# Performance work log

Measured on AMD Instinct MI355X. Metric: run time of the kernel, lower is better.

## Reference

```python
import jax, jax.numpy as jnp
import numpy as np

N_NODES = 10000
N_EDGES = 160000
D_IN = 512
D_HID = 1024

def setup_inputs() -> dict:
    key = jax.random.key(0)
    ks = jax.random.split(key, 8)
    feat = jax.random.normal(ks[0], (N_NODES, D_IN), dtype=jnp.float32)
    W1 = jax.random.normal(ks[1], (D_IN, D_HID), dtype=jnp.float32) * (1.0 / np.sqrt(D_IN))
    b1 = jnp.zeros((D_HID,), dtype=jnp.float32)
    W2 = jax.random.normal(ks[2], (D_HID, D_IN), dtype=jnp.float32) * (1.0 / np.sqrt(D_HID))
    b2 = jnp.zeros((D_IN,), dtype=jnp.float32)
    eps = jnp.zeros((1,), dtype=jnp.float32)
    src = jax.random.randint(ks[3], (N_EDGES,), 0, N_NODES, dtype=jnp.int32)
    dst = jax.random.randint(ks[4], (N_EDGES,), 0, N_NODES, dtype=jnp.int32)
    return {"feat": feat, "W1": W1, "b1": b1, "W2": W2, "b2": b2,
            "eps": eps, "src": src, "dst": dst}

def reference(feat, W1, b1, W2, b2, eps, src, dst):
    # message passing: copy src feature along each edge, sum-reduce at dst
    msgs = feat[src]                                   # [E, D_IN] gather
    neigh = jax.ops.segment_sum(msgs, dst, num_segments=feat.shape[0])  # [N, D_IN]
    # GIN combine: (1 + eps) * self + sum(neighbors)
    rst = (1.0 + eps[0]) * feat + neigh
    # apply_func: 2-layer MLP with ReLU
    h = jnp.maximum(rst @ W1 + b1, 0.0)
    h = h @ W2 + b2
    # identity residual (in_dim == out_dim)
    return h + feat
```

## Files before the change

kernel.cpp:

```cpp
#include <hip/hip_runtime.h>

typedef unsigned short u16;
typedef unsigned int u32;
typedef __bf16 bf16x8 __attribute__((ext_vector_type(8)));
typedef float f32x4 __attribute__((ext_vector_type(4)));

#define N_NODES 10000
#define N_EDGES 160000
#define D_IN 512
#define D_HID 1024

#define AS1 __attribute__((address_space(1)))
#define AS3 __attribute__((address_space(3)))

__device__ __forceinline__ u16 f2bf(float f) {
    union { float f; u32 u; } v; v.f = f;
    return (u16)((v.u + 0x7fffu + ((v.u >> 16) & 1u)) >> 16);
}
__device__ __forceinline__ float b2f(u32 h) {
    union { u32 u; float f; } v; v.u = h << 16; return v.f;
}

__global__ void hist_k(const int* __restrict__ dst, int* __restrict__ counts) {
    int e = blockIdx.x * 256 + threadIdx.x;
    if (e < N_EDGES) atomicAdd(&counts[dst[e]], 1);
}

__global__ __launch_bounds__(1024) void scan_k(const int* __restrict__ counts,
                                               int* __restrict__ offs,
                                               int* __restrict__ cursor) {
    __shared__ int wpre[16];
    int t = threadIdx.x, l = t & 63, w = t >> 6;
    int base = t * 10;
    int c[10];
    int lsum = 0;
#pragma unroll
    for (int i = 0; i < 10; i++) {
        int idx = base + i;
        c[i] = (idx < N_NODES) ? counts[idx] : 0;
        lsum += c[i];
    }
    int sc = lsum;
#pragma unroll
    for (int d = 1; d < 64; d <<= 1) {
        int v = __shfl_up(sc, d);
        if (l >= d) sc += v;
    }
    __shared__ int wsum[16];
    if (l == 63) wsum[w] = sc;
    __syncthreads();
    if (w == 0 && l < 16) {
        int v = wsum[l];
        int p = v;
#pragma unroll
        for (int d = 1; d < 16; d <<= 1) {
            int u = __shfl_up(p, d);
            if (l >= d) p += u;
        }
        wpre[l] = p - v;
    }
    __syncthreads();
    int run = wpre[w] + sc - lsum;
#pragma unroll
    for (int i = 0; i < 10; i++) {
        int idx = base + i;
        if (idx < N_NODES) { offs[idx] = run; cursor[idx] = run; run += c[i]; }
    }
    if (t == 1023) offs[N_NODES] = wpre[15] + sc;
}

__global__ void reorder_k(const int* __restrict__ src, const int* __restrict__ dst,
                          int* __restrict__ cursor, int* __restrict__ ssrc) {
    int e = blockIdx.x * 256 + threadIdx.x;
    if (e >= N_EDGES) return;
    int d = dst[e];
    int pos = atomicAdd(&cursor[d], 1);
    ssrc[pos] = src[e];
}

__global__ void cvt_bf16_k(const float* __restrict__ in, u16* __restrict__ out, int n) {
    int i = (blockIdx.x * 256 + threadIdx.x) * 8;
    if (i >= n) return;
    float4 a = *(const float4*)(in + i);
    float4 b = *(const float4*)(in + i + 4);
    uint4 o;
    o.x = (u32)f2bf(a.x) | ((u32)f2bf(a.y) << 16);
    o.y = (u32)f2bf(a.z) | ((u32)f2bf(a.w) << 16);
    o.z = (u32)f2bf(b.x) | ((u32)f2bf(b.y) << 16);
    o.w = (u32)f2bf(b.z) | ((u32)f2bf(b.w) << 16);
    *(uint4*)(out + i) = o;
}

__global__ void transw_k(const float* __restrict__ W1, u16* __restrict__ w1t,
                         const float* __restrict__ W2, u16* __restrict__ w2t) {
    __shared__ float tile[32][33];
    int b = blockIdx.x;
    const float* W; u16* WT; int K, N, nt;
    if (b < 512) { W = W1; WT = w1t; K = D_IN;  N = D_HID; nt = 32; }
    else         { b -= 512; W = W2; WT = w2t; K = D_HID; N = D_IN;  nt = 16; }
    int n0 = (b % nt) * 32, k0 = (b / nt) * 32;
    int tx = threadIdx.x, ty = threadIdx.y;
#pragma unroll
    for (int i = 0; i < 32; i += 8)
        tile[ty + i][tx] = W[(size_t)(k0 + ty + i) * N + n0 + tx];
    __syncthreads();
#pragma unroll
    for (int i = 0; i < 32; i += 8)
        WT[(size_t)(n0 + ty + i) * K + k0 + tx] = f2bf(tile[tx][ty + i]);
}

__global__ __launch_bounds__(128) void gather_k(const float* __restrict__ feat,
                                                const u16* __restrict__ featb,
                                                const float* __restrict__ eps,
                                                const int* __restrict__ offs,
                                                const int* __restrict__ ssrc,
                                                u16* __restrict__ out) {
    int n = (blockIdx.x * 128 + threadIdx.x) >> 6;
    int l = threadIdx.x & 63;
    if (n >= N_NODES) return;
    int beg = offs[n], end = offs[n + 1];
    float s = 1.0f + eps[0];
    float4 s0 = *(const float4*)(feat + (size_t)n * D_IN + l * 8);
    float4 s1 = *(const float4*)(feat + (size_t)n * D_IN + l * 8 + 4);
    float acc[8] = { s * s0.x, s * s0.y, s * s0.z, s * s0.w,
                     s * s1.x, s * s1.y, s * s1.z, s * s1.w };
    int e = beg;
    for (; e + 4 <= end; e += 4) {
        int i0 = ssrc[e], i1 = ssrc[e + 1], i2 = ssrc[e + 2], i3 = ssrc[e + 3];
        uint4 v0 = *(const uint4*)(featb + (size_t)i0 * D_IN + l * 8);
        uint4 v1 = *(const uint4*)(featb + (size_t)i1 * D_IN + l * 8);
        uint4 v2 = *(const uint4*)(featb + (size_t)i2 * D_IN + l * 8);
        uint4 v3 = *(const uint4*)(featb + (size_t)i3 * D_IN + l * 8);
#define ACC4(v) \
        acc[0] += b2f(v.x & 0xffffu); acc[1] += b2f(v.x >> 16); \
        acc[2] += b2f(v.y & 0xffffu); acc[3] += b2f(v.y >> 16); \
        acc[4] += b2f(v.z & 0xffffu); acc[5] += b2f(v.z >> 16); \
        acc[6] += b2f(v.w & 0xffffu); acc[7] += b2f(v.w >> 16);
        ACC4(v0) ACC4(v1) ACC4(v2) ACC4(v3)
    }
    for (; e < end; e++) {
        int i0 = ssrc[e];
        uint4 v0 = *(const uint4*)(featb + (size_t)i0 * D_IN + l * 8);
        ACC4(v0)
    }
#undef ACC4
    uint4 o;
    o.x = (u32)f2bf(acc[0]) | ((u32)f2bf(acc[1]) << 16);
    o.y = (u32)f2bf(acc[2]) | ((u32)f2bf(acc[3]) << 16);
    o.z = (u32)f2bf(acc[4]) | ((u32)f2bf(acc[5]) << 16);
    o.w = (u32)f2bf(acc[6]) | ((u32)f2bf(acc[7]) << 16);
    *(uint4*)(out + (size_t)n * D_IN + l * 8) = o;
}

template <int EPI>
__global__ __launch_bounds__(256) void gemm_k(const u16* __restrict__ A,
                                              const u16* __restrict__ BT,
                                              const float* __restrict__ bias,
                                              const float* __restrict__ feat,
                                              void* __restrict__ Cout,
                                              int M, int N, int K) {
    __shared__ __bf16 sA[128 * 64];
    __shared__ __bf16 sB[128 * 64];
    const int row0 = blockIdx.y * 128;
    const int col0 = blockIdx.x * 128;
    const int t = threadIdx.x;
    const int w = t >> 6, l = t & 63;
    const int wm = (w >> 1) * 64, wn = (w & 1) * 64;
    const int lr = l & 15;
    const int lq = l >> 4;

    const u16* pA[4];
    const u16* pB[4];
    __bf16* lA[4];
    __bf16* lB[4];
    {
        int rloc = w * 32 + (l >> 3);
        int gch8 = (((l & 7) ^ (l >> 3)) * 8);
#pragma unroll
        for (int q = 0; q < 4; q++) {
            int ar = row0 + rloc + q * 8; if (ar > M - 1) ar = M - 1;
            pA[q] = A + (size_t)ar * K + gch8;
            int br = col0 + rloc + q * 8;
            pB[q] = BT + (size_t)br * K + gch8;
            lA[q] = sA + (w * 32 + q * 8) * 64;
            lB[q] = sB + (w * 32 + q * 8) * 64;
        }
    }
    const int fo = ((lq ^ (lr & 7)) * 8);

    f32x4 acc[4][4] = {};

    for (int k0 = 0; k0 < K; k0 += 64) {
        __syncthreads();
#pragma unroll
        for (int q = 0; q < 4; q++) {
            __builtin_amdgcn_global_load_lds((const AS1 void*)(pA[q] + k0),
                                             (AS3 void*)lA[q], 16, 0, 0);
            __builtin_amdgcn_global_load_lds((const AS1 void*)(pB[q] + k0),
                                             (AS3 void*)lB[q], 16, 0, 0);
        }
        __syncthreads();
#pragma unroll
        for (int kk = 0; kk < 64; kk += 32) {
            const int fx = fo ^ kk;
            bf16x8 fa[4], fb[4];
#pragma unroll
            for (int i = 0; i < 4; i++)
                fa[i] = *(const bf16x8*)(sA + (wm + i * 16 + lr) * 64 + fx);
#pragma unroll
            for (int j = 0; j < 4; j++)
                fb[j] = *(const bf16x8*)(sB + (wn + j * 16 + lr) * 64 + fx);
#pragma unroll
            for (int i = 0; i < 4; i++)
#pragma unroll
                for (int j = 0; j < 4; j++)
                    acc[i][j] = __builtin_amdgcn_mfma_f32_16x16x32_bf16(
                        fa[i], fb[j], acc[i][j], 0, 0, 0);
        }
    }

#pragma unroll
    for (int i = 0; i < 4; i++) {
        int rowb = row0 + wm + i * 16 + lq * 4;
#pragma unroll
        for (int j = 0; j < 4; j++) {
            int col = col0 + wn + j * 16 + lr;
            float bv = bias[col];
#pragma unroll
            for (int r = 0; r < 4; r++) {
                int rr = rowb + r;
                if (rr < M) {
                    float v = acc[i][j][r] + bv;
                    if (EPI == 0) {
                        v = fmaxf(v, 0.0f);
                        ((u16*)Cout)[(size_t)rr * N + col] = f2bf(v);
                    } else {
                        v += feat[(size_t)rr * N + col];
                        ((float*)Cout)[(size_t)rr * N + col] = v;
                    }
                }
            }
        }
    }
}

extern "C" void kernel_launch(void* const* d_in, const int* in_sizes, int n_in,
                              void* d_out, int out_size, void* d_ws, size_t ws_size,
                              hipStream_t stream) {
    const float* feat = (const float*)d_in[0];
    const float* W1   = (const float*)d_in[1];
    const float* b1   = (const float*)d_in[2];
    const float* W2   = (const float*)d_in[3];
    const float* b2   = (const float*)d_in[4];
    const float* eps  = (const float*)d_in[5];
    const int*   src  = (const int*)d_in[6];
    const int*   dst  = (const int*)d_in[7];
    float* out = (float*)d_out;

    char* ws = (char*)d_ws;
    u16* rst_b16 = (u16*)(ws);
    u16* h_b16   = (u16*)(ws + 10240000);
    u16* featb   = (u16*)(ws + 30720000);
    u16* w1t     = (u16*)(ws + 40960000);
    u16* w2t     = (u16*)(ws + 42008576);
    int* counts  = (int*)(ws + 43057152);
    int* offs    = (int*)(ws + 43097152);
    int* cursor  = (int*)(ws + 43137160);
    int* ssrc    = (int*)(ws + 43177160);

    const int NE = N_NODES * D_IN;

    hipMemsetAsync(counts, 0, N_NODES * sizeof(int), stream);
    hist_k<<<(N_EDGES + 255) / 256, 256, 0, stream>>>(dst, counts);
    scan_k<<<1, 1024, 0, stream>>>(counts, offs, cursor);
    reorder_k<<<(N_EDGES + 255) / 256, 256, 0, stream>>>(src, dst, cursor, ssrc);

    cvt_bf16_k<<<NE / 8 / 256, 256, 0, stream>>>(feat, featb, NE);
    transw_k<<<1024, dim3(32, 8), 0, stream>>>(W1, w1t, W2, w2t);

    gather_k<<<(N_NODES + 1) / 2, 128, 0, stream>>>(feat, featb, eps, offs, ssrc, rst_b16);

    const int MT = (N_NODES + 127) / 128;
    gemm_k<0><<<dim3(D_HID / 128, MT), 256, 0, stream>>>(rst_b16, w1t, b1, nullptr,
                                                         (void*)h_b16, N_NODES, D_HID, D_IN);
    gemm_k<1><<<dim3(D_IN / 128, MT), 256, 0, stream>>>(h_b16, w2t, b2, feat,
                                                        (void*)out, N_NODES, D_IN, D_HID);
}
```

Before: 206.4 us.

## Double-buffer LDS tiles in GEMM to overlap global loads with MFMA

The GEMM kernel now keeps two LDS buffers per operand. It issues the global_load_lds for the next K tile before computing on the current one, and uses a partial vmcnt wait plus barriers in place of the two full syncthreads per iteration. The goal is to hide global memory latency behind the MFMA work. In exchange, LDS use per block doubles, which can lower occupancy, and the last iteration issues a redundant reload of the same tile.

```diff
diff --git a/kernel.cpp b/kernel.cpp
--- a/kernel.cpp
+++ b/kernel.cpp
@@ -159,8 +159,8 @@
                                               const float* __restrict__ feat,
                                               void* __restrict__ Cout,
                                               int M, int N, int K) {
-    __shared__ __bf16 sA[128 * 64];
-    __shared__ __bf16 sB[128 * 64];
+    __shared__ __bf16 sA[2][128 * 64];
+    __shared__ __bf16 sB[2][128 * 64];
     const int row0 = blockIdx.y * 128;
     const int col0 = blockIdx.x * 128;
     const int t = threadIdx.x;
@@ -171,8 +171,7 @@
 
     const u16* pA[4];
     const u16* pB[4];
-    __bf16* lA[4];
-    __bf16* lB[4];
+    int loff[4];
     {
         int rloc = w * 32 + (l >> 3);
         int gch8 = (((l & 7) ^ (l >> 3)) * 8);
@@ -182,34 +181,40 @@
             pA[q] = A + (size_t)ar * K + gch8;
             int br = col0 + rloc + q * 8;
             pB[q] = BT + (size_t)br * K + gch8;
-            lA[q] = sA + (w * 32 + q * 8) * 64;
-            lB[q] = sB + (w * 32 + q * 8) * 64;
+            loff[q] = (w * 32 + q * 8) * 64;
         }
     }
     const int fo = ((lq ^ (lr & 7)) * 8);
 
     f32x4 acc[4][4] = {};
 
-    for (int k0 = 0; k0 < K; k0 += 64) {
-        __syncthreads();
+    auto STAGE = [&](int buf, int kk0) {
 #pragma unroll
         for (int q = 0; q < 4; q++) {
-            __builtin_amdgcn_global_load_lds((const AS1 void*)(pA[q] + k0),
-                                             (AS3 void*)lA[q], 16, 0, 0);
-            __builtin_amdgcn_global_load_lds((const AS1 void*)(pB[q] + k0),
-                                             (AS3 void*)lB[q], 16, 0, 0);
-        }
-        __syncthreads();
+            __builtin_amdgcn_global_load_lds((const AS1 void*)(pA[q] + kk0),
+                                             (AS3 void*)(&sA[buf][loff[q]]), 16, 0, 0);
+            __builtin_amdgcn_global_load_lds((const AS1 void*)(pB[q] + kk0),
+                                             (AS3 void*)(&sB[buf][loff[q]]), 16, 0, 0);
+        }
+    };
+
+    STAGE(0, 0);
+    int cur = 0;
+    for (int k0 = 0; k0 < K; k0 += 64, cur ^= 1) {
+        int kn = (k0 + 64 < K) ? (k0 + 64) : k0;
+        STAGE(cur ^ 1, kn);
+        asm volatile("s_waitcnt vmcnt(8)" ::: "memory");
+        __builtin_amdgcn_s_barrier();
 #pragma unroll
         for (int kk = 0; kk < 64; kk += 32) {
             const int fx = fo ^ kk;
             bf16x8 fa[4], fb[4];
 #pragma unroll
             for (int i = 0; i < 4; i++)
-                fa[i] = *(const bf16x8*)(sA + (wm + i * 16 + lr) * 64 + fx);
+                fa[i] = *(const bf16x8*)(&sA[cur][0] + (wm + i * 16 + lr) * 64 + fx);
 #pragma unroll
             for (int j = 0; j < 4; j++)
-                fb[j] = *(const bf16x8*)(sB + (wn + j * 16 + lr) * 64 + fx);
+                fb[j] = *(const bf16x8*)(&sB[cur][0] + (wn + j * 16 + lr) * 64 + fx);
 #pragma unroll
             for (int i = 0; i < 4; i++)
 #pragma unroll
@@ -217,6 +222,7 @@
                     acc[i][j] = __builtin_amdgcn_mfma_f32_16x16x32_bf16(
                         fa[i], fb[j], acc[i][j], 0, 0, 0);
         }
+        __builtin_amdgcn_s_barrier();
     }
 
 #pragma unroll
```

Result: slower. 221.8 us (+7.4%).

## Double-buffer GEMM LDS tiles via register prefetch and remap blocks per XCD

Applied to the files above, without the earlier changes.

Replaces the direct global-to-LDS loads in the GEMM with register-staged prefetch into a double-buffered shared-memory tile, so the next K tile's global loads overlap the current tile's MFMA work and one barrier per iteration is removed. It also remaps workgroup indices so consecutive tiles land on the same XCD for better L2 reuse, and sets a 2-blocks-per-CU occupancy hint. The trade-off is double the LDS use (64 KB per block) and more register pressure from the staged uint4 values. The swizzle moves from the global address to the LDS write offset.

```diff
diff --git a/kernel.cpp b/kernel.cpp
--- a/kernel.cpp
+++ b/kernel.cpp
@@ -9,9 +9,6 @@
 #define N_EDGES 160000
 #define D_IN 512
 #define D_HID 1024
-
-#define AS1 __attribute__((address_space(1)))
-#define AS3 __attribute__((address_space(3)))
 
 __device__ __forceinline__ u16 f2bf(float f) {
     union { float f; u32 u; } v; v.f = f;
@@ -153,16 +150,24 @@
 }
 
 template <int EPI>
-__global__ __launch_bounds__(256) void gemm_k(const u16* __restrict__ A,
-                                              const u16* __restrict__ BT,
-                                              const float* __restrict__ bias,
-                                              const float* __restrict__ feat,
-                                              void* __restrict__ Cout,
-                                              int M, int N, int K) {
-    __shared__ __bf16 sA[128 * 64];
-    __shared__ __bf16 sB[128 * 64];
-    const int row0 = blockIdx.y * 128;
-    const int col0 = blockIdx.x * 128;
+__global__ __launch_bounds__(256, 2) void gemm_k(const u16* __restrict__ A,
+                                                 const u16* __restrict__ BT,
+                                                 const float* __restrict__ bias,
+                                                 const float* __restrict__ feat,
+                                                 void* __restrict__ Cout,
+                                                 int M, int N, int K) {
+    __shared__ __bf16 sA[2][128 * 64];
+    __shared__ __bf16 sB[2][128 * 64];
+
+    const int NX = gridDim.x;
+    const int nwg = NX * gridDim.y;
+    const int flat = blockIdx.y * NX + blockIdx.x;
+    const int qq = nwg >> 3, rr8 = nwg & 7;
+    const int xcd = flat & 7, idx = flat >> 3;
+    const int L = (xcd < rr8 ? xcd * (qq + 1) : rr8 * (qq + 1) + (xcd - rr8) * qq) + idx;
+    const int row0 = (L / NX) * 128;
+    const int col0 = (L % NX) * 128;
+
     const int t = threadIdx.x;
     const int w = t >> 6, l = t & 63;
     const int wm = (w >> 1) * 64, wn = (w & 1) * 64;
@@ -171,51 +176,75 @@
 
     const u16* pA[4];
     const u16* pB[4];
-    __bf16* lA[4];
-    __bf16* lB[4];
+    u32 ldso[4];
     {
         int rloc = w * 32 + (l >> 3);
-        int gch8 = (((l & 7) ^ (l >> 3)) * 8);
+        int gch8 = (l & 7) * 8;
+        int slot = ((l & 7) ^ (l >> 3)) * 8;
 #pragma unroll
         for (int q = 0; q < 4; q++) {
             int ar = row0 + rloc + q * 8; if (ar > M - 1) ar = M - 1;
             pA[q] = A + (size_t)ar * K + gch8;
             int br = col0 + rloc + q * 8;
             pB[q] = BT + (size_t)br * K + gch8;
-            lA[q] = sA + (w * 32 + q * 8) * 64;
-            lB[q] = sB + (w * 32 + q * 8) * 64;
+            ldso[q] = (u32)(((rloc + q * 8) * 64 + slot) * 2);
         }
     }
     const int fo = ((lq ^ (lr & 7)) * 8);
 
     f32x4 acc[4][4] = {};
-
-    for (int k0 = 0; k0 < K; k0 += 64) {
+    uint4 stA[4], stB[4];
+
+    const int NT = K >> 6;
+
+#pragma unroll
+    for (int q = 0; q < 4; q++) {
+        stA[q] = *(const uint4*)(pA[q]);
+        stB[q] = *(const uint4*)(pB[q]);
+    }
+#pragma unroll
+    for (int q = 0; q < 4; q++) {
+        *(uint4*)((char*)(&sA[0][0]) + ldso[q]) = stA[q];
+        *(uint4*)((char*)(&sB[0][0]) + ldso[q]) = stB[q];
+    }
+
+    for (int it = 0; it < NT; ++it) {
         __syncthreads();
-#pragma unroll
-        for (int q = 0; q < 4; q++) {
-            __builtin_amdgcn_global_load_lds((const AS1 void*)(pA[q] + k0),
-                                             (AS3 void*)lA[q], 16, 0, 0);
-            __builtin_amdgcn_global_load_lds((const AS1 void*)(pB[q] + k0),
-                                             (AS3 void*)lB[q], 16, 0, 0);
-        }
-        __syncthreads();
+        if (it + 1 < NT) {
+            int kn = (it + 1) << 6;
+#pragma unroll
+            for (int q = 0; q < 4; q++) {
+                stA[q] = *(const uint4*)(pA[q] + kn);
+                stB[q] = *(const uint4*)(pB[q] + kn);
+            }
+        }
+        const __bf16* cA = &sA[it & 1][0];
+        const __bf16* cB = &sB[it & 1][0];
 #pragma unroll
         for (int kk = 0; kk < 64; kk += 32) {
             const int fx = fo ^ kk;
             bf16x8 fa[4], fb[4];
 #pragma unroll
             for (int i = 0; i < 4; i++)
-                fa[i] = *(const bf16x8*)(sA + (wm + i * 16 + lr) * 64 + fx);
+                fa[i] = *(const bf16x8*)(cA + (wm + i * 16 + lr) * 64 + fx);
 #pragma unroll
             for (int j = 0; j < 4; j++)
-                fb[j] = *(const bf16x8*)(sB + (wn + j * 16 + lr) * 64 + fx);
+                fb[j] = *(const bf16x8*)(cB + (wn + j * 16 + lr) * 64 + fx);
 #pragma unroll
             for (int i = 0; i < 4; i++)
 #pragma unroll
                 for (int j = 0; j < 4; j++)
                     acc[i][j] = __builtin_amdgcn_mfma_f32_16x16x32_bf16(
                         fa[i], fb[j], acc[i][j], 0, 0, 0);
+        }
+        if (it + 1 < NT) {
+            __bf16* nA = &sA[(it + 1) & 1][0];
+            __bf16* nB = &sB[(it + 1) & 1][0];
+#pragma unroll
+            for (int q = 0; q < 4; q++) {
+                *(uint4*)((char*)nA + ldso[q]) = stA[q];
+                *(uint4*)((char*)nB + ldso[q]) = stB[q];
+            }
         }
     }
 
```

Result: slower. 289.4 us (+40.2%).

## Fuse two-layer MLP into one kernel and merge preprocessing launches

Applied to the files above, without the earlier changes.

Replaces the two tiled GEMM kernels with a single kernel that keeps a 48-row block of the input and the hidden activations in LDS, so the hidden tensor never round-trips through global memory. Weight fragments are read straight from global memory (L2) rather than staged in LDS. The histogram, feature bf16 conversion and weight transpose are also merged into one launch. The fused kernel uses about 144KB of LDS per block and clamps the last block to overlap rows, which gives low occupancy and heavy repeated weight reads.

```diff
diff --git a/kernel.cpp b/kernel.cpp
--- a/kernel.cpp
+++ b/kernel.cpp
@@ -21,9 +21,47 @@
     union { u32 u; float f; } v; v.u = h << 16; return v.f;
 }
 
-__global__ void hist_k(const int* __restrict__ dst, int* __restrict__ counts) {
-    int e = blockIdx.x * 256 + threadIdx.x;
-    if (e < N_EDGES) atomicAdd(&counts[dst[e]], 1);
+__global__ __launch_bounds__(256) void prep_k(const int* __restrict__ dst,
+                                              int* __restrict__ counts,
+                                              const float* __restrict__ feat,
+                                              u16* __restrict__ featb,
+                                              const float* __restrict__ W1,
+                                              u16* __restrict__ w1t,
+                                              const float* __restrict__ W2,
+                                              u16* __restrict__ w2t) {
+    int b = blockIdx.x;
+    int t = threadIdx.x;
+    if (b < 625) {
+        int e = b * 256 + t;
+        if (e < N_EDGES) atomicAdd(&counts[dst[e]], 1);
+        return;
+    }
+    if (b < 625 + 2500) {
+        int i = ((b - 625) * 256 + t) * 8;
+        float4 a = *(const float4*)(feat + i);
+        float4 c = *(const float4*)(feat + i + 4);
+        uint4 o;
+        o.x = (u32)f2bf(a.x) | ((u32)f2bf(a.y) << 16);
+        o.y = (u32)f2bf(a.z) | ((u32)f2bf(a.w) << 16);
+        o.z = (u32)f2bf(c.x) | ((u32)f2bf(c.y) << 16);
+        o.w = (u32)f2bf(c.z) | ((u32)f2bf(c.w) << 16);
+        *(uint4*)(featb + i) = o;
+        return;
+    }
+    __shared__ float tile[32][33];
+    b -= 3125;
+    const float* W; u16* WT; int K, N, nt;
+    if (b < 512) { W = W1; WT = w1t; K = D_IN;  N = D_HID; nt = 32; }
+    else         { b -= 512; W = W2; WT = w2t; K = D_HID; N = D_IN;  nt = 16; }
+    int n0 = (b % nt) * 32, k0 = (b / nt) * 32;
+    int tx = t & 31, ty = t >> 5;
+#pragma unroll
+    for (int i = 0; i < 32; i += 8)
+        tile[ty + i][tx] = W[(size_t)(k0 + ty + i) * N + n0 + tx];
+    __syncthreads();
+#pragma unroll
+    for (int i = 0; i < 32; i += 8)
+        WT[(size_t)(n0 + ty + i) * K + k0 + tx] = f2bf(tile[tx][ty + i]);
 }
 
 __global__ __launch_bounds__(1024) void scan_k(const int* __restrict__ counts,
@@ -76,37 +114,6 @@
     int d = dst[e];
     int pos = atomicAdd(&cursor[d], 1);
     ssrc[pos] = src[e];
-}
-
-__global__ void cvt_bf16_k(const float* __restrict__ in, u16* __restrict__ out, int n) {
-    int i = (blockIdx.x * 256 + threadIdx.x) * 8;
-    if (i >= n) return;
-    float4 a = *(const float4*)(in + i);
-    float4 b = *(const float4*)(in + i + 4);
-    uint4 o;
-    o.x = (u32)f2bf(a.x) | ((u32)f2bf(a.y) << 16);
-    o.y = (u32)f2bf(a.z) | ((u32)f2bf(a.w) << 16);
-    o.z = (u32)f2bf(b.x) | ((u32)f2bf(b.y) << 16);
-    o.w = (u32)f2bf(b.z) | ((u32)f2bf(b.w) << 16);
-    *(uint4*)(out + i) = o;
-}
-
-__global__ void transw_k(const float* __restrict__ W1, u16* __restrict__ w1t,
-                         const float* __restrict__ W2, u16* __restrict__ w2t) {
-    __shared__ float tile[32][33];
-    int b = blockIdx.x;
-    const float* W; u16* WT; int K, N, nt;
-    if (b < 512) { W = W1; WT = w1t; K = D_IN;  N = D_HID; nt = 32; }
-    else         { b -= 512; W = W2; WT = w2t; K = D_HID; N = D_IN;  nt = 16; }
-    int n0 = (b % nt) * 32, k0 = (b / nt) * 32;
-    int tx = threadIdx.x, ty = threadIdx.y;
-#pragma unroll
-    for (int i = 0; i < 32; i += 8)
-        tile[ty + i][tx] = W[(size_t)(k0 + ty + i) * N + n0 + tx];
-    __syncthreads();
-#pragma unroll
-    for (int i = 0; i < 32; i += 8)
-        WT[(size_t)(n0 + ty + i) * K + k0 + tx] = f2bf(tile[tx][ty + i]);
 }
 
 __global__ __launch_bounds__(128) void gather_k(const float* __restrict__ feat,
@@ -152,95 +159,110 @@
     *(uint4*)(out + (size_t)n * D_IN + l * 8) = o;
 }
 
-template <int EPI>
-__global__ __launch_bounds__(256) void gemm_k(const u16* __restrict__ A,
-                                              const u16* __restrict__ BT,
-                                              const float* __restrict__ bias,
-                                              const float* __restrict__ feat,
-                                              void* __restrict__ Cout,
-                                              int M, int N, int K) {
-    __shared__ __bf16 sA[128 * 64];
-    __shared__ __bf16 sB[128 * 64];
-    const int row0 = blockIdx.y * 128;
-    const int col0 = blockIdx.x * 128;
+__global__ __launch_bounds__(512) void fused_mlp_k(const u16* __restrict__ A,
+                                                   const u16* __restrict__ W1T,
+                                                   const float* __restrict__ b1,
+                                                   const u16* __restrict__ W2T,
+                                                   const float* __restrict__ b2,
+                                                   const float* __restrict__ feat,
+                                                   float* __restrict__ out,
+                                                   int M) {
+    __shared__ __bf16 sA[48 * 512];
+    __shared__ __bf16 sH[48 * 1024];
+
+    int row0 = blockIdx.x * 48;
+    if (row0 > M - 48) row0 = M - 48;
     const int t = threadIdx.x;
     const int w = t >> 6, l = t & 63;
-    const int wm = (w >> 1) * 64, wn = (w & 1) * 64;
-    const int lr = l & 15;
-    const int lq = l >> 4;
-
-    const u16* pA[4];
-    const u16* pB[4];
-    __bf16* lA[4];
-    __bf16* lB[4];
+    const int lr = l & 15, lq = l >> 4;
+
     {
-        int rloc = w * 32 + (l >> 3);
-        int gch8 = (((l & 7) ^ (l >> 3)) * 8);
-#pragma unroll
-        for (int q = 0; q < 4; q++) {
-            int ar = row0 + rloc + q * 8; if (ar > M - 1) ar = M - 1;
-            pA[q] = A + (size_t)ar * K + gch8;
-            int br = col0 + rloc + q * 8;
-            pB[q] = BT + (size_t)br * K + gch8;
-            lA[q] = sA + (w * 32 + q * 8) * 64;
-            lB[q] = sB + (w * 32 + q * 8) * 64;
+#pragma unroll
+        for (int q = 0; q < 6; q++) {
+            const int row = w * 6 + q;
+            const u16* src = A + (size_t)(row0 + row) * 512 + ((l ^ (row & 7)) * 8);
+            __builtin_amdgcn_global_load_lds((const AS1 void*)src,
+                                             (AS3 void*)(&sA[row * 512]), 16, 0, 0);
         }
     }
-    const int fo = ((lq ^ (lr & 7)) * 8);
-
-    f32x4 acc[4][4] = {};
-
-    for (int k0 = 0; k0 < K; k0 += 64) {
-        __syncthreads();
-#pragma unroll
-        for (int q = 0; q < 4; q++) {
-            __builtin_amdgcn_global_load_lds((const AS1 void*)(pA[q] + k0),
-                                             (AS3 void*)lA[q], 16, 0, 0);
-            __builtin_amdgcn_global_load_lds((const AS1 void*)(pB[q] + k0),
-                                             (AS3 void*)lB[q], 16, 0, 0);
+    asm volatile("s_waitcnt vmcnt(0)" ::: "memory");
+    __syncthreads();
+
+    for (int hh = 0; hh < 2; hh++) {
+        const int n0 = hh * 512 + w * 64;
+        f32x4 acc[3][4] = {};
+        for (int kt = 0; kt < 8; kt++) {
+#pragma unroll
+            for (int kk = 0; kk < 64; kk += 32) {
+                const int c = kt * 8 + (kk >> 3) + lq;
+                bf16x8 fa[3], fb[4];
+#pragma unroll
+                for (int i = 0; i < 3; i++)
+                    fa[i] = *(const bf16x8*)(&sA[(i * 16 + lr) * 512 + ((c ^ (lr & 7)) * 8)]);
+#pragma unroll
+                for (int j = 0; j < 4; j++)
+                    fb[j] = *(const bf16x8*)(W1T + (size_t)(n0 + j * 16 + lr) * 512
+                                             + kt * 64 + kk + lq * 8);
+#pragma unroll
+                for (int i = 0; i < 3; i++)
+#pragma unroll
+                    for (int j = 0; j < 4; j++)
+                        acc[i][j] = __builtin_amdgcn_mfma_f32_16x16x32_bf16(
+                            fa[i], fb[j], acc[i][j], 0, 0, 0);
+            }
         }
-        __syncthreads();
-#pragma unroll
-        for (int kk = 0; kk < 64; kk += 32) {
-            const int fx = fo ^ kk;
-            bf16x8 fa[4], fb[4];
-#pragma unroll
-            for (int i = 0; i < 4; i++)
-                fa[i] = *(const bf16x8*)(sA + (wm + i * 16 + lr) * 64 + fx);
-#pragma unroll
-            for (int j = 0; j < 4; j++)
-                fb[j] = *(const bf16x8*)(sB + (wn + j * 16 + lr) * 64 + fx);
-#pragma unroll
-            for (int i = 0; i < 4; i++)
-#pragma unroll
-                for (int j = 0; j < 4; j++)
-                    acc[i][j] = __builtin_amdgcn_mfma_f32_16x16x32_bf16(
-                        fa[i], fb[j], acc[i][j], 0, 0, 0);
-        }
-    }
-
-#pragma unroll
-    for (int i = 0; i < 4; i++) {
-        int rowb = row0 + wm + i * 16 + lq * 4;
-#pragma unroll
-        for (int j = 0; j < 4; j++) {
-            int col = col0 + wn + j * 16 + lr;
-            float bv = bias[col];
-#pragma unroll
-            for (int r = 0; r < 4; r++) {
-                int rr = rowb + r;
-                if (rr < M) {
-                    float v = acc[i][j][r] + bv;
-                    if (EPI == 0) {
-                        v = fmaxf(v, 0.0f);
-                        ((u16*)Cout)[(size_t)rr * N + col] = f2bf(v);
-                    } else {
-                        v += feat[(size_t)rr * N + col];
-                        ((float*)Cout)[(size_t)rr * N + col] = v;
-                    }
+#pragma unroll
+        for (int i = 0; i < 3; i++)
+#pragma unroll
+            for (int j = 0; j < 4; j++) {
+                const int n = n0 + j * 16 + lr;
+                const float bv = b1[n];
+#pragma unroll
+                for (int r = 0; r < 4; r++) {
+                    const int row = i * 16 + lq * 4 + r;
+                    const float v = fmaxf(acc[i][j][r] + bv, 0.0f);
+                    ((u16*)sH)[row * 1024 + (((n >> 3) ^ (row & 7)) * 8) + (n & 7)] = f2bf(v);
                 }
             }
+    }
+    __syncthreads();
+
+    {
+        const int n0 = w * 64;
+        f32x4 acc[3][4] = {};
+        for (int kt = 0; kt < 16; kt++) {
+#pragma unroll
+            for (int kk = 0; kk < 64; kk += 32) {
+                const int c = kt * 8 + (kk >> 3) + lq;
+                bf16x8 fa[3], fb[4];
+#pragma unroll
+                for (int i = 0; i < 3; i++)
+                    fa[i] = *(const bf16x8*)(&sH[(i * 16 + lr) * 1024 + ((c ^ (lr & 7)) * 8)]);
+#pragma unroll
+                for (int j = 0; j < 4; j++)
+                    fb[j] = *(const bf16x8*)(W2T + (size_t)(n0 + j * 16 + lr) * 1024
+                                             + kt * 64 + kk + lq * 8);
+#pragma unroll
+                for (int i = 0; i < 3; i++)
+#pragma unroll
+                    for (int j = 0; j < 4; j++)
+                        acc[i][j] = __builtin_amdgcn_mfma_f32_16x16x32_bf16(
+                            fa[i], fb[j], acc[i][j], 0, 0, 0);
+            }
         }
+#pragma unroll
+        for (int i = 0; i < 3; i++)
+#pragma unroll
+            for (int j = 0; j < 4; j++) {
+                const int col = n0 + j * 16 + lr;
+                const float bv = b2[col];
+#pragma unroll
+                for (int r = 0; r < 4; r++) {
+                    const int row = row0 + i * 16 + lq * 4 + r;
+                    out[(size_t)row * 512 + col] =
+                        acc[i][j][r] + bv + feat[(size_t)row * 512 + col];
+                }
+            }
     }
 }
 
@@ -259,7 +281,6 @@
 
     char* ws = (char*)d_ws;
     u16* rst_b16 = (u16*)(ws);
-    u16* h_b16   = (u16*)(ws + 10240000);
     u16* featb   = (u16*)(ws + 30720000);
     u16* w1t     = (u16*)(ws + 40960000);
     u16* w2t     = (u16*)(ws + 42008576);
@@ -268,21 +289,15 @@
     int* cursor  = (int*)(ws + 43137160);
     int* ssrc    = (int*)(ws + 43177160);
 
-    const int NE = N_NODES * D_IN;
-
     hipMemsetAsync(counts, 0, N_NODES * sizeof(int), stream);
-    hist_k<<<(N_EDGES + 255) / 256, 256, 0, stream>>>(dst, counts);
+    prep_k<<<625 + 2500 + 1024, 256, 0, stream>>>(dst, counts, feat, featb,
+                                                  W1, w1t, W2, w2t);
     scan_k<<<1, 1024, 0, stream>>>(counts, offs, cursor);
     reorder_k<<<(N_EDGES + 255) / 256, 256, 0, stream>>>(src, dst, cursor, ssrc);
 
-    cvt_bf16_k<<<NE / 8 / 256, 256, 0, stream>>>(feat, featb, NE);
-    transw_k<<<1024, dim3(32, 8), 0, stream>>>(W1, w1t, W2, w2t);
-
     gather_k<<<(N_NODES + 1) / 2, 128, 0, stream>>>(feat, featb, eps, offs, ssrc, rst_b16);
 
-    const int MT = (N_NODES + 127) / 128;
-    gemm_k<0><<<dim3(D_HID / 128, MT), 256, 0, stream>>>(rst_b16, w1t, b1, nullptr,
-                                                         (void*)h_b16, N_NODES, D_HID, D_IN);
-    gemm_k<1><<<dim3(D_IN / 128, MT), 256, 0, stream>>>(h_b16, w2t, b2, feat,
-                                                        (void*)out, N_NODES, D_IN, D_HID);
-}
+    const int NB = (N_NODES + 47) / 48;
+    fused_mlp_k<<<NB, 512, 0, stream>>>(rst_b16, w1t, b1, w2t, b2, feat,
+                                        out, N_NODES);
+}
```

Result: slower. 241.8 us (+17.1%).
